# Kernel tuning notes

Hardware: AMD Instinct MI355X
Metric: run time of the kernel (lower is better)

## Reference

```python
import jax, jax.numpy as jnp
import numpy as np

B, S, D, H = 2, 2048, 1024, 16
DEPTH = D // H


def setup_inputs() -> dict:
    key = jax.random.key(0)
    ks = jax.random.split(key, 12)
    sc = 1.0 / np.sqrt(D)
    n = lambda k, shp, s=sc: jax.random.normal(k, shp, dtype=jnp.float32) * s
    return {
        "q": jax.random.normal(ks[0], (B, S, D), dtype=jnp.float32),
        "k": jax.random.normal(ks[1], (B, S, D), dtype=jnp.float32),
        "v": jax.random.normal(ks[2], (B, S, D), dtype=jnp.float32),
        # key-padding mask: 1 = masked, 0 = keep (added to logits * -1e9)
        "mask": (jax.random.uniform(ks[3], (B, 1, 1, S)) < 0.1).astype(jnp.float32),
        "wq_w": n(ks[4], (D, D)), "wq_b": jnp.zeros((D,), jnp.float32),
        "wk_w": n(ks[5], (D, D)), "wk_b": jnp.zeros((D,), jnp.float32),
        "wv_w": n(ks[6], (D, D)), "wv_b": jnp.zeros((D,), jnp.float32),
        "dense_w": n(ks[7], (D, D)), "dense_b": jnp.zeros((D,), jnp.float32),
    }


def _split_heads(x, b, s):
    # [B, S, D] -> [B, H, S, depth]
    return x.reshape(b, s, H, DEPTH).transpose(0, 2, 1, 3)


def reference(q, k, v, mask, wq_w, wq_b, wk_w, wk_b, wv_w, wv_b, dense_w, dense_b):
    b, sq, _ = q.shape
    sk = k.shape[1]
    qh = _split_heads(q @ wq_w.T + wq_b, b, sq)
    kh = _split_heads(k @ wk_w.T + wk_b, b, sk)
    vh = _split_heads(v @ wv_w.T + wv_b, b, sk)
    scale = 1.0 / jnp.sqrt(jnp.float32(DEPTH))
    logits = jnp.einsum('bhqd,bhkd->bhqk', qh, kh) * scale  # [B,H,Sq,Sk]
    logits = logits + mask * (-1e9)
    attn = jax.nn.softmax(logits, axis=-1)
    ctx = jnp.einsum('bhqk,bhkd->bhqd', attn, vh)
    ctx = ctx.transpose(0, 2, 1, 3).reshape(b, sq, D)  # concat heads
    out = ctx @ dense_w.T + dense_b
    return out, attn
```

## Files before the change

kernel.cpp:

```cpp
#include <hip/hip_runtime.h>

#define BB 2
#define SS 2048
#define DD 1024
#define HH 16
#define DEPTH 64
#define MTOT (BB*SS)
#define QW 8
#define QBLK (QW*16)
#define NT (SS/64)
#define NPROJ ((size_t)BB*HH*SS*DEPTH)
#define WSZ   ((size_t)DD*DD)

using f16 = _Float16;
typedef _Float16 f16x8 __attribute__((ext_vector_type(8)));
typedef _Float16 f16x4 __attribute__((ext_vector_type(4)));
typedef float f32x4 __attribute__((ext_vector_type(4)));

#define LOG2E 1.44269504088896f
#define SC2   (0.125f * LOG2E)

#define GLOAD16(g, l) __builtin_amdgcn_global_load_lds(                      \
    (__attribute__((address_space(1))) const void*)(g),                      \
    (__attribute__((address_space(3))) void*)(l), 16, 0, 0)

__global__ __launch_bounds__(256) void cvt_kernel(
    const float* __restrict__ q, const float* __restrict__ k, const float* __restrict__ v,
    const float* __restrict__ w0, const float* __restrict__ w1, const float* __restrict__ w2,
    f16* __restrict__ qf, f16* __restrict__ kf, f16* __restrict__ vf,
    f16* __restrict__ wq, f16* __restrict__ wk, f16* __restrict__ wv)
{
    const int z = blockIdx.y;
    const float* s = z==0?q : z==1?k : z==2?v : z==3?w0 : z==4?w1 : w2;
    f16*        d = z==0?qf: z==1?kf: z==2?vf: z==3?wq: z==4?wk: wv;
    const size_t n = (z < 3) ? NPROJ : WSZ;
    for (size_t i = ((size_t)blockIdx.x * 256 + threadIdx.x) * 8; i < n;
         i += (size_t)gridDim.x * 256 * 8) {
        f32x4 a = *(const f32x4*)(s + i);
        f32x4 b = *(const f32x4*)(s + i + 4);
        f16x8 o = {(f16)a[0], (f16)a[1], (f16)a[2], (f16)a[3],
                   (f16)b[0], (f16)b[1], (f16)b[2], (f16)b[3]};
        *(f16x8*)(d + i) = o;
    }
}

__global__ __launch_bounds__(256) void cvt2_kernel(
    const float* __restrict__ s, f16* __restrict__ d)
{
    size_t i = ((size_t)blockIdx.x * 256 + threadIdx.x) * 8;
    if (i < WSZ) {
        f32x4 a = *(const f32x4*)(s + i);
        f32x4 b = *(const f32x4*)(s + i + 4);
        f16x8 o = {(f16)a[0], (f16)a[1], (f16)a[2], (f16)a[3],
                   (f16)b[0], (f16)b[1], (f16)b[2], (f16)b[3]};
        *(f16x8*)(d + i) = o;
    }
}

__global__ __launch_bounds__(256) void proj_kernel(
    const f16* __restrict__ qf, const f16* __restrict__ kf, const f16* __restrict__ vf,
    const f16* __restrict__ wqw, const f16* __restrict__ wkw, const f16* __restrict__ wvw,
    const float* __restrict__ bq, const float* __restrict__ bk, const float* __restrict__ bv,
    f16* __restrict__ qh, f16* __restrict__ kh, f16* __restrict__ vt)
{
    const int mode = blockIdx.z;
    const f16* A    = mode==0 ? qf  : mode==1 ? kf  : vf;
    const f16* Bw   = mode==0 ? wqw : mode==1 ? wkw : wvw;
    const float* bias = mode==0 ? bq : mode==1 ? bk : bv;

    __shared__ f16 As[128*64];
    __shared__ f16 Bs[128*64];

    const int tid = threadIdx.x, wave = tid >> 6, lane = tid & 63;
    const int m0 = blockIdx.y * 128, n0 = blockIdx.x * 128;
    const int wm = (wave >> 1) * 64, wn = (wave & 1) * 64;
    const int lrow = lane & 15, g = lane >> 4;
    const int sw = lrow & 7;
    const int srow = tid >> 3;
    const int schk = (tid & 7) ^ (srow & 7);

    f32x4 acc[4][4] = {};

    for (int kk = 0; kk < DD; kk += 64) {
        #pragma unroll
        for (int i = 0; i < 4; ++i) {
            GLOAD16(A  + (size_t)(m0 + i*32 + srow) * DD + kk + schk * 8,
                    &As[i*2048 + wave*512]);
            GLOAD16(Bw + (size_t)(n0 + i*32 + srow) * DD + kk + schk * 8,
                    &Bs[i*2048 + wave*512]);
        }
        __syncthreads();
        for (int kf2 = 0; kf2 < 2; ++kf2) {
            f16x8 a[4], bf[4];
            for (int i = 0; i < 4; ++i)
                a[i]  = *(const f16x8*)&As[(wm + i*16 + lrow)*64 + ((kf2*4 + g) ^ sw)*8];
            for (int i = 0; i < 4; ++i)
                bf[i] = *(const f16x8*)&Bs[(wn + i*16 + lrow)*64 + ((kf2*4 + g) ^ sw)*8];
            for (int mi = 0; mi < 4; ++mi)
                for (int ni = 0; ni < 4; ++ni)
                    acc[mi][ni] = __builtin_amdgcn_mfma_f32_16x16x32_f16(a[mi], bf[ni], acc[mi][ni], 0, 0, 0);
        }
        __syncthreads();
    }

    const int rbase = g * 4;
    if (mode == 2) {
        for (int ni = 0; ni < 4; ++ni) {
            int n = n0 + wn + ni * 16 + lrow;
            float bval = bias[n];
            int hh = n >> 6, dep = n & 63;
            for (int mi = 0; mi < 4; ++mi) {
                int m = m0 + wm + mi * 16 + rbase;
                int bb = m >> 11, s = m & 2047;
                f16x4 pk = {(f16)(acc[mi][ni][0] + bval), (f16)(acc[mi][ni][1] + bval),
                            (f16)(acc[mi][ni][2] + bval), (f16)(acc[mi][ni][3] + bval)};
                *(f16x4*)&vt[((size_t)(bb * HH + hh) * DEPTH + dep) * SS + s] = pk;
            }
        }
    } else {
        f16* dst = (mode == 0) ? qh : kh;
        for (int ni = 0; ni < 4; ++ni) {
            int n = n0 + wn + ni * 16 + lrow;
            float bval = bias[n];
            int hh = n >> 6, dep = n & 63;
            for (int mi = 0; mi < 4; ++mi)
                for (int j = 0; j < 4; ++j) {
                    int m = m0 + wm + mi * 16 + rbase + j;
                    int bb = m >> 11, s = m & 2047;
                    dst[((size_t)(bb * HH + hh) * SS + s) * DEPTH + dep] = (f16)(acc[mi][ni][j] + bval);
                }
        }
    }
}

__global__ __launch_bounds__(512) void attn_kernel(
    const f16* __restrict__ qh, const f16* __restrict__ kh, const f16* __restrict__ vt,
    const float* __restrict__ mask, float* __restrict__ attn_out, f16* __restrict__ ctx)
{
    __shared__ float mlds[SS];
    __shared__ f16 Ks[2][64*64];
    __shared__ f16 Vs[2][64*64];
    __shared__ f16 Pl[QW][16][72];

    const int tid = threadIdx.x, wave = tid >> 6, lane = tid & 63;
    const int L = blockIdx.x;
    const int xcd = L & 7, iw = L >> 3;
    const int bh = xcd * 4 + (iw >> 4);
    const int qb = iw & 15;
    const int b = bh >> 4, h = bh & 15;
    const int q0 = qb * QBLK;
    const int lrow = lane & 15, g = lane >> 4;
    const int rbase = g * 4;
    const int sw = lrow & 7;
    const int srow = tid >> 3;
    const int schk = (tid & 7) ^ (srow & 7);

    const f16* Qbase = qh + (size_t)bh * SS * DEPTH;
    const f16* Kb = kh + (size_t)bh * SS * DEPTH;
    const f16* Vb = vt + (size_t)bh * DEPTH * SS;

    for (int i = tid; i < SS; i += 512) mlds[i] = mask[b * SS + i] * (-1e9f * LOG2E);

    f16x8 aq[2];
    for (int kf2 = 0; kf2 < 2; ++kf2)
        aq[kf2] = *(const f16x8*)(Qbase + (size_t)(q0 + wave*16 + lrow) * DEPTH + kf2*32 + g*8);

    float s_l[4] = {0.f, 0.f, 0.f, 0.f};
    GLOAD16(Kb + (size_t)(0*64 + srow) * DEPTH + schk * 8, &Ks[0][wave * 512]);
    __syncthreads();
    for (int kt = 0; kt < NT; ++kt) {
        const int cur = kt & 1;
        if (kt + 1 < NT)
            GLOAD16(Kb + (size_t)((kt+1)*64 + srow) * DEPTH + schk * 8, &Ks[cur ^ 1][wave * 512]);
        for (int nf = 0; nf < 4; ++nf) {
            f32x4 a4 = {};
            for (int kf2 = 0; kf2 < 2; ++kf2) {
                f16x8 bf = *(const f16x8*)&Ks[cur][(nf*16 + lrow)*64 + ((kf2*4 + g) ^ sw)*8];
                a4 = __builtin_amdgcn_mfma_f32_16x16x32_f16(aq[kf2], bf, a4, 0, 0, 0);
            }
            float mb = mlds[kt*64 + nf*16 + lrow];
            for (int j = 0; j < 4; ++j)
                s_l[j] += __builtin_amdgcn_exp2f(a4[j] * SC2 + mb);
        }
        __syncthreads();
    }
    for (int j = 0; j < 4; ++j) {
        float s = s_l[j];
        for (int off = 1; off < 16; off <<= 1) s += __shfl_xor(s, off);
        s_l[j] = 1.0f / s;
    }

    f32x4 cacc[4] = {};
    float* arow = attn_out + ((size_t)bh * SS + q0 + wave * 16) * SS;
    GLOAD16(Kb + (size_t)(0*64 + srow) * DEPTH + schk * 8, &Ks[0][wave * 512]);
    GLOAD16(Vb + (size_t)srow * SS + 0*64 + schk * 8,      &Vs[0][wave * 512]);
    __syncthreads();
    for (int kt = 0; kt < NT; ++kt) {
        const int cur = kt & 1;
        if (kt + 1 < NT) {
            GLOAD16(Kb + (size_t)((kt+1)*64 + srow) * DEPTH + schk * 8, &Ks[cur ^ 1][wave * 512]);
            GLOAD16(Vb + (size_t)srow * SS + (kt+1)*64 + schk * 8,      &Vs[cur ^ 1][wave * 512]);
        }
        for (int nf = 0; nf < 4; ++nf) {
            f32x4 a4 = {};
            for (int kf2 = 0; kf2 < 2; ++kf2) {
                f16x8 bf = *(const f16x8*)&Ks[cur][(nf*16 + lrow)*64 + ((kf2*4 + g) ^ sw)*8];
                a4 = __builtin_amdgcn_mfma_f32_16x16x32_f16(aq[kf2], bf, a4, 0, 0, 0);
            }
            float mb = mlds[kt*64 + nf*16 + lrow];
            for (int j = 0; j < 4; ++j) {
                float p = __builtin_amdgcn_exp2f(a4[j] * SC2 + mb) * s_l[j];
                Pl[wave][rbase + j][nf*16 + lrow] = (f16)p;
            }
        }
        for (int i = 0; i < 4; ++i) {
            int r = i * 4 + g;
            f16x4 pv4 = *(const f16x4*)&Pl[wave][r][lrow * 4];
            f32x4 o = {(float)pv4[0], (float)pv4[1], (float)pv4[2], (float)pv4[3]};
            __builtin_nontemporal_store(o, (f32x4*)&arow[(size_t)r * SS + kt*64 + lrow*4]);
        }
        for (int kf2 = 0; kf2 < 2; ++kf2) {
            f16x8 pa = *(const f16x8*)&Pl[wave][lrow][kf2*32 + g*8];
            for (int nf = 0; nf < 4; ++nf) {
                f16x8 bv = *(const f16x8*)&Vs[cur][(nf*16 + lrow)*64 + ((kf2*4 + g) ^ sw)*8];
                cacc[nf] = __builtin_amdgcn_mfma_f32_16x16x32_f16(pa, bv, cacc[nf], 0, 0, 0);
            }
        }
        __syncthreads();
    }
    for (int nf = 0; nf < 4; ++nf)
        for (int j = 0; j < 4; ++j) {
            int qrow = q0 + wave * 16 + rbase + j;
            ctx[((size_t)(b * SS + qrow) * HH + h) * DEPTH + nf*16 + lrow] = (f16)cacc[nf][j];
        }
}

__global__ __launch_bounds__(256) void dense_kernel(
    const f16* __restrict__ ctx, const f16* __restrict__ W16,
    const float* __restrict__ bias, float* __restrict__ out)
{
    __shared__ f16 As[128*64];
    __shared__ f16 Bs[128*64];

    const int tid = threadIdx.x, wave = tid >> 6, lane = tid & 63;
    const int m0 = blockIdx.y * 128, n0 = blockIdx.x * 128;
    const int wm = (wave >> 1) * 64, wn = (wave & 1) * 64;
    const int lrow = lane & 15, g = lane >> 4;
    const int sw = lrow & 7;
    const int srow = tid >> 3;
    const int schk = (tid & 7) ^ (srow & 7);

    f32x4 acc[4][4] = {};

    for (int kk = 0; kk < DD; kk += 64) {
        #pragma unroll
        for (int i = 0; i < 4; ++i) {
            GLOAD16(ctx + (size_t)(m0 + i*32 + srow) * DD + kk + schk * 8,
                    &As[i*2048 + wave*512]);
            GLOAD16(W16 + (size_t)(n0 + i*32 + srow) * DD + kk + schk * 8,
                    &Bs[i*2048 + wave*512]);
        }
        __syncthreads();
        for (int kf2 = 0; kf2 < 2; ++kf2) {
            f16x8 a[4], bf[4];
            for (int i = 0; i < 4; ++i)
                a[i]  = *(const f16x8*)&As[(wm + i*16 + lrow)*64 + ((kf2*4 + g) ^ sw)*8];
            for (int i = 0; i < 4; ++i)
                bf[i] = *(const f16x8*)&Bs[(wn + i*16 + lrow)*64 + ((kf2*4 + g) ^ sw)*8];
            for (int mi = 0; mi < 4; ++mi)
                for (int ni = 0; ni < 4; ++ni)
                    acc[mi][ni] = __builtin_amdgcn_mfma_f32_16x16x32_f16(a[mi], bf[ni], acc[mi][ni], 0, 0, 0);
        }
        __syncthreads();
    }

    const int rbase = g * 4;
    for (int ni = 0; ni < 4; ++ni) {
        int n = n0 + wn + ni * 16 + lrow;
        float bval = bias[n];
        for (int mi = 0; mi < 4; ++mi)
            for (int j = 0; j < 4; ++j) {
                int m = m0 + wm + mi * 16 + rbase + j;
                out[(size_t)m * DD + n] = acc[mi][ni][j] + bval;
            }
    }
}

extern "C" void kernel_launch(void* const* d_in, const int* in_sizes, int n_in,
                              void* d_out, int out_size, void* d_ws, size_t ws_size,
                              hipStream_t stream) {
    const float* q       = (const float*)d_in[0];
    const float* k       = (const float*)d_in[1];
    const float* v       = (const float*)d_in[2];
    const float* mask    = (const float*)d_in[3];
    const float* wq_w    = (const float*)d_in[4];
    const float* wq_b    = (const float*)d_in[5];
    const float* wk_w    = (const float*)d_in[6];
    const float* wk_b    = (const float*)d_in[7];
    const float* wv_w    = (const float*)d_in[8];
    const float* wv_b    = (const float*)d_in[9];
    const float* dense_w = (const float*)d_in[10];
    const float* dense_b = (const float*)d_in[11];

    float* out  = (float*)d_out;
    float* attn = out + (size_t)MTOT * DD;

    f16* qh  = (f16*)d_ws;
    f16* kh  = qh + NPROJ;
    f16* vt  = kh + NPROJ;
    f16* ctx = vt + NPROJ;

    f16* sc   = (f16*)attn;
    f16* qf   = sc;
    f16* kf   = sc + NPROJ;
    f16* vf   = sc + 2*NPROJ;
    f16* wq16 = sc + 3*NPROJ;
    f16* wk16 = wq16 + WSZ;
    f16* wv16 = wk16 + WSZ;

    f16* dw16 = qh;

    cvt_kernel<<<dim3(1024, 6), 256, 0, stream>>>(q, k, v, wq_w, wk_w, wv_w,
                                                  qf, kf, vf, wq16, wk16, wv16);
    proj_kernel<<<dim3(8, 32, 3), 256, 0, stream>>>(qf, kf, vf, wq16, wk16, wv16,
                                                    wq_b, wk_b, wv_b, qh, kh, vt);
    attn_kernel<<<dim3(512), 512, 0, stream>>>(qh, kh, vt, mask, attn, ctx);
    cvt2_kernel<<<dim3(512), 256, 0, stream>>>(dense_w, dw16);
    dense_kernel<<<dim3(8, 32), 256, 0, stream>>>(ctx, dw16, dense_b, out);
}
```

Baseline: 235.6 us.

## Double-buffer GEMM K-tiles and defer attention-probability stores by one tile

The projection and dense GEMMs switch from single-buffered 64-wide K tiles to double-buffered 32-wide K tiles with a new XOR swizzle. The next tile's async global-to-LDS load is issued before computing on the current one, so load latency overlaps the MFMA work. In the attention kernel, the fp32 attention-probability stores for a tile are held in registers and issued at the start of the next iteration, so they overlap the following loads and MFMAs. The cost is more registers, a barrier every 32 K instead of every 64, and a swizzle change that must still avoid LDS bank conflicts.

Measured after the change: 244.0 us. +3.6%, slower.

```diff
diff --git a/kernel.cpp b/kernel.cpp
--- a/kernel.cpp
+++ b/kernel.cpp
@@ -68,38 +68,45 @@
     const f16* Bw   = mode==0 ? wqw : mode==1 ? wkw : wvw;
     const float* bias = mode==0 ? bq : mode==1 ? bk : bv;
 
-    __shared__ f16 As[128*64];
-    __shared__ f16 Bs[128*64];
+    __shared__ f16 As[2][128*32];
+    __shared__ f16 Bs[2][128*32];
 
     const int tid = threadIdx.x, wave = tid >> 6, lane = tid & 63;
     const int m0 = blockIdx.y * 128, n0 = blockIdx.x * 128;
     const int wm = (wave >> 1) * 64, wn = (wave & 1) * 64;
     const int lrow = lane & 15, g = lane >> 4;
-    const int sw = lrow & 7;
-    const int srow = tid >> 3;
-    const int schk = (tid & 7) ^ (srow & 7);
+    const int swr = (lrow >> 1) & 3;
+    const int srow = tid >> 2;
+    const int schk = (tid & 3) ^ ((tid >> 3) & 3);
 
     f32x4 acc[4][4] = {};
 
-    for (int kk = 0; kk < DD; kk += 64) {
-        #pragma unroll
-        for (int i = 0; i < 4; ++i) {
-            GLOAD16(A  + (size_t)(m0 + i*32 + srow) * DD + kk + schk * 8,
-                    &As[i*2048 + wave*512]);
-            GLOAD16(Bw + (size_t)(n0 + i*32 + srow) * DD + kk + schk * 8,
-                    &Bs[i*2048 + wave*512]);
-        }
-        __syncthreads();
-        for (int kf2 = 0; kf2 < 2; ++kf2) {
-            f16x8 a[4], bf[4];
-            for (int i = 0; i < 4; ++i)
-                a[i]  = *(const f16x8*)&As[(wm + i*16 + lrow)*64 + ((kf2*4 + g) ^ sw)*8];
-            for (int i = 0; i < 4; ++i)
-                bf[i] = *(const f16x8*)&Bs[(wn + i*16 + lrow)*64 + ((kf2*4 + g) ^ sw)*8];
-            for (int mi = 0; mi < 4; ++mi)
-                for (int ni = 0; ni < 4; ++ni)
-                    acc[mi][ni] = __builtin_amdgcn_mfma_f32_16x16x32_f16(a[mi], bf[ni], acc[mi][ni], 0, 0, 0);
-        }
+    auto stage = [&](int t, int buf) {
+        const int kk = t * 32;
+        #pragma unroll
+        for (int s2 = 0; s2 < 2; ++s2) {
+            GLOAD16(A  + (size_t)(m0 + s2*64 + srow) * DD + kk + schk * 8,
+                    &As[buf][s2*2048 + wave*512]);
+            GLOAD16(Bw + (size_t)(n0 + s2*64 + srow) * DD + kk + schk * 8,
+                    &Bs[buf][s2*2048 + wave*512]);
+        }
+    };
+
+    stage(0, 0);
+    __syncthreads();
+    for (int t = 0; t < DD/32; ++t) {
+        const int cur = t & 1;
+        if (t + 1 < DD/32) stage(t + 1, cur ^ 1);
+        f16x8 a[4], bf[4];
+        #pragma unroll
+        for (int i = 0; i < 4; ++i)
+            a[i]  = *(const f16x8*)&As[cur][(wm + i*16 + lrow)*32 + (g ^ swr)*8];
+        #pragma unroll
+        for (int i = 0; i < 4; ++i)
+            bf[i] = *(const f16x8*)&Bs[cur][(wn + i*16 + lrow)*32 + (g ^ swr)*8];
+        for (int mi = 0; mi < 4; ++mi)
+            for (int ni = 0; ni < 4; ++ni)
+                acc[mi][ni] = __builtin_amdgcn_mfma_f32_16x16x32_f16(a[mi], bf[ni], acc[mi][ni], 0, 0, 0);
         __syncthreads();
     }
 
@@ -191,12 +198,21 @@
     }
 
     f32x4 cacc[4] = {};
+    f32x4 st[4];
     float* arow = attn_out + ((size_t)bh * SS + q0 + wave * 16) * SS;
     GLOAD16(Kb + (size_t)(0*64 + srow) * DEPTH + schk * 8, &Ks[0][wave * 512]);
     GLOAD16(Vb + (size_t)srow * SS + 0*64 + schk * 8,      &Vs[0][wave * 512]);
     __syncthreads();
     for (int kt = 0; kt < NT; ++kt) {
         const int cur = kt & 1;
+        if (kt > 0) {
+            #pragma unroll
+            for (int i = 0; i < 4; ++i) {
+                int r = i * 4 + g;
+                __builtin_nontemporal_store(st[i],
+                    (f32x4*)&arow[(size_t)r * SS + (kt-1)*64 + lrow*4]);
+            }
+        }
         if (kt + 1 < NT) {
             GLOAD16(Kb + (size_t)((kt+1)*64 + srow) * DEPTH + schk * 8, &Ks[cur ^ 1][wave * 512]);
             GLOAD16(Vb + (size_t)srow * SS + (kt+1)*64 + schk * 8,      &Vs[cur ^ 1][wave * 512]);
@@ -213,12 +229,6 @@
                 Pl[wave][rbase + j][nf*16 + lrow] = (f16)p;
             }
         }
-        for (int i = 0; i < 4; ++i) {
-            int r = i * 4 + g;
-            f16x4 pv4 = *(const f16x4*)&Pl[wave][r][lrow * 4];
-            f32x4 o = {(float)pv4[0], (float)pv4[1], (float)pv4[2], (float)pv4[3]};
-            __builtin_nontemporal_store(o, (f32x4*)&arow[(size_t)r * SS + kt*64 + lrow*4]);
-        }
         for (int kf2 = 0; kf2 < 2; ++kf2) {
             f16x8 pa = *(const f16x8*)&Pl[wave][lrow][kf2*32 + g*8];
             for (int nf = 0; nf < 4; ++nf) {
@@ -226,7 +236,19 @@
                 cacc[nf] = __builtin_amdgcn_mfma_f32_16x16x32_f16(pa, bv, cacc[nf], 0, 0, 0);
             }
         }
+        #pragma unroll
+        for (int i = 0; i < 4; ++i) {
+            int r = i * 4 + g;
+            f16x4 pv4 = *(const f16x4*)&Pl[wave][r][lrow * 4];
+            st[i] = (f32x4){(float)pv4[0], (float)pv4[1], (float)pv4[2], (float)pv4[3]};
+        }
         __syncthreads();
+    }
+    #pragma unroll
+    for (int i = 0; i < 4; ++i) {
+        int r = i * 4 + g;
+        __builtin_nontemporal_store(st[i],
+            (f32x4*)&arow[(size_t)r * SS + (NT-1)*64 + lrow*4]);
     }
     for (int nf = 0; nf < 4; ++nf)
         for (int j = 0; j < 4; ++j) {
@@ -239,38 +261,45 @@
     const f16* __restrict__ ctx, const f16* __restrict__ W16,
     const float* __restrict__ bias, float* __restrict__ out)
 {
-    __shared__ f16 As[128*64];
-    __shared__ f16 Bs[128*64];
+    __shared__ f16 As[2][128*32];
+    __shared__ f16 Bs[2][128*32];
 
     const int tid = threadIdx.x, wave = tid >> 6, lane = tid & 63;
     const int m0 = blockIdx.y * 128, n0 = blockIdx.x * 128;
     const int wm = (wave >> 1) * 64, wn = (wave & 1) * 64;
     const int lrow = lane & 15, g = lane >> 4;
-    const int sw = lrow & 7;
-    const int srow = tid >> 3;
-    const int schk = (tid & 7) ^ (srow & 7);
+    const int swr = (lrow >> 1) & 3;
+    const int srow = tid >> 2;
+    const int schk = (tid & 3) ^ ((tid >> 3) & 3);
 
     f32x4 acc[4][4] = {};
 
-    for (int kk = 0; kk < DD; kk += 64) {
-        #pragma unroll
-        for (int i = 0; i < 4; ++i) {
-            GLOAD16(ctx + (size_t)(m0 + i*32 + srow) * DD + kk + schk * 8,
-                    &As[i*2048 + wave*512]);
-            GLOAD16(W16 + (size_t)(n0 + i*32 + srow) * DD + kk + schk * 8,
-                    &Bs[i*2048 + wave*512]);
-        }
-        __syncthreads();
-        for (int kf2 = 0; kf2 < 2; ++kf2) {
-            f16x8 a[4], bf[4];
-            for (int i = 0; i < 4; ++i)
-                a[i]  = *(const f16x8*)&As[(wm + i*16 + lrow)*64 + ((kf2*4 + g) ^ sw)*8];
-            for (int i = 0; i < 4; ++i)
-                bf[i] = *(const f16x8*)&Bs[(wn + i*16 + lrow)*64 + ((kf2*4 + g) ^ sw)*8];
-            for (int mi = 0; mi < 4; ++mi)
-                for (int ni = 0; ni < 4; ++ni)
-                    acc[mi][ni] = __builtin_amdgcn_mfma_f32_16x16x32_f16(a[mi], bf[ni], acc[mi][ni], 0, 0, 0);
-        }
+    auto stage = [&](int t, int buf) {
+        const int kk = t * 32;
+        #pragma unroll
+        for (int s2 = 0; s2 < 2; ++s2) {
+            GLOAD16(ctx + (size_t)(m0 + s2*64 + srow) * DD + kk + schk * 8,
+                    &As[buf][s2*2048 + wave*512]);
+            GLOAD16(W16 + (size_t)(n0 + s2*64 + srow) * DD + kk + schk * 8,
+                    &Bs[buf][s2*2048 + wave*512]);
+        }
+    };
+
+    stage(0, 0);
+    __syncthreads();
+    for (int t = 0; t < DD/32; ++t) {
+        const int cur = t & 1;
+        if (t + 1 < DD/32) stage(t + 1, cur ^ 1);
+        f16x8 a[4], bf[4];
+        #pragma unroll
+        for (int i = 0; i < 4; ++i)
+            a[i]  = *(const f16x8*)&As[cur][(wm + i*16 + lrow)*32 + (g ^ swr)*8];
+        #pragma unroll
+        for (int i = 0; i < 4; ++i)
+            bf[i] = *(const f16x8*)&Bs[cur][(wn + i*16 + lrow)*32 + (g ^ swr)*8];
+        for (int mi = 0; mi < 4; ++mi)
+            for (int ni = 0; ni < 4; ++ni)
+                acc[mi][ni] = __builtin_amdgcn_mfma_f32_16x16x32_f16(a[mi], bf[ni], acc[mi][ni], 0, 0, 0);
         __syncthreads();
     }
 
```

## Defer attention-probability stores one tile and shrink mask to byte flags

Applied to the files above, without the earlier changes.

The attention kernel now reads each tile's probabilities back from LDS after the PV MFMAs into registers, and issues the fp32 nontemporal global stores at the start of the next iteration, so the HBM writes overlap the following tile's compute. The fp32 mask bias array in LDS is replaced by a byte flag array with a multiplicative 0/1 select, which cuts LDS use. The launch bounds also gain a min-blocks hint of 6, which pressures register allocation. The deferred stores keep 16 extra registers live, and masked positions give exactly zero instead of exp of a huge negative value. That matches the reference in practice, though rows with every key masked would behave differently.

Result: no change. 235.2 us (-0.2%).

```diff
diff --git a/kernel.cpp b/kernel.cpp
--- a/kernel.cpp
+++ b/kernel.cpp
@@ -133,11 +133,11 @@
     }
 }
 
-__global__ __launch_bounds__(512) void attn_kernel(
+__global__ __launch_bounds__(512, 6) void attn_kernel(
     const f16* __restrict__ qh, const f16* __restrict__ kh, const f16* __restrict__ vt,
     const float* __restrict__ mask, float* __restrict__ attn_out, f16* __restrict__ ctx)
 {
-    __shared__ float mlds[SS];
+    __shared__ unsigned char mflag[SS];
     __shared__ f16 Ks[2][64*64];
     __shared__ f16 Vs[2][64*64];
     __shared__ f16 Pl[QW][16][72];
@@ -159,7 +159,8 @@
     const f16* Kb = kh + (size_t)bh * SS * DEPTH;
     const f16* Vb = vt + (size_t)bh * DEPTH * SS;
 
-    for (int i = tid; i < SS; i += 512) mlds[i] = mask[b * SS + i] * (-1e9f * LOG2E);
+    for (int i = tid; i < SS; i += 512)
+        mflag[i] = mask[b * SS + i] > 0.5f ? 1 : 0;
 
     f16x8 aq[2];
     for (int kf2 = 0; kf2 < 2; ++kf2)
@@ -178,9 +179,9 @@
                 f16x8 bf = *(const f16x8*)&Ks[cur][(nf*16 + lrow)*64 + ((kf2*4 + g) ^ sw)*8];
                 a4 = __builtin_amdgcn_mfma_f32_16x16x32_f16(aq[kf2], bf, a4, 0, 0, 0);
             }
-            float mb = mlds[kt*64 + nf*16 + lrow];
+            float sel = mflag[kt*64 + nf*16 + lrow] ? 0.f : 1.f;
             for (int j = 0; j < 4; ++j)
-                s_l[j] += __builtin_amdgcn_exp2f(a4[j] * SC2 + mb);
+                s_l[j] += sel * __builtin_amdgcn_exp2f(a4[j] * SC2);
         }
         __syncthreads();
     }
@@ -191,12 +192,21 @@
     }
 
     f32x4 cacc[4] = {};
+    f32x4 st[4];
     float* arow = attn_out + ((size_t)bh * SS + q0 + wave * 16) * SS;
     GLOAD16(Kb + (size_t)(0*64 + srow) * DEPTH + schk * 8, &Ks[0][wave * 512]);
     GLOAD16(Vb + (size_t)srow * SS + 0*64 + schk * 8,      &Vs[0][wave * 512]);
     __syncthreads();
     for (int kt = 0; kt < NT; ++kt) {
         const int cur = kt & 1;
+        if (kt > 0) {
+            #pragma unroll
+            for (int i = 0; i < 4; ++i) {
+                int r = i * 4 + g;
+                __builtin_nontemporal_store(st[i],
+                    (f32x4*)&arow[(size_t)r * SS + (kt-1)*64 + lrow*4]);
+            }
+        }
         if (kt + 1 < NT) {
             GLOAD16(Kb + (size_t)((kt+1)*64 + srow) * DEPTH + schk * 8, &Ks[cur ^ 1][wave * 512]);
             GLOAD16(Vb + (size_t)srow * SS + (kt+1)*64 + schk * 8,      &Vs[cur ^ 1][wave * 512]);
@@ -207,17 +217,11 @@
                 f16x8 bf = *(const f16x8*)&Ks[cur][(nf*16 + lrow)*64 + ((kf2*4 + g) ^ sw)*8];
                 a4 = __builtin_amdgcn_mfma_f32_16x16x32_f16(aq[kf2], bf, a4, 0, 0, 0);
             }
-            float mb = mlds[kt*64 + nf*16 + lrow];
+            float sel = mflag[kt*64 + nf*16 + lrow] ? 0.f : 1.f;
             for (int j = 0; j < 4; ++j) {
-                float p = __builtin_amdgcn_exp2f(a4[j] * SC2 + mb) * s_l[j];
+                float p = sel * __builtin_amdgcn_exp2f(a4[j] * SC2) * s_l[j];
                 Pl[wave][rbase + j][nf*16 + lrow] = (f16)p;
             }
-        }
-        for (int i = 0; i < 4; ++i) {
-            int r = i * 4 + g;
-            f16x4 pv4 = *(const f16x4*)&Pl[wave][r][lrow * 4];
-            f32x4 o = {(float)pv4[0], (float)pv4[1], (float)pv4[2], (float)pv4[3]};
-            __builtin_nontemporal_store(o, (f32x4*)&arow[(size_t)r * SS + kt*64 + lrow*4]);
         }
         for (int kf2 = 0; kf2 < 2; ++kf2) {
             f16x8 pa = *(const f16x8*)&Pl[wave][lrow][kf2*32 + g*8];
@@ -226,7 +230,19 @@
                 cacc[nf] = __builtin_amdgcn_mfma_f32_16x16x32_f16(pa, bv, cacc[nf], 0, 0, 0);
             }
         }
-        __syncthreads();
+        #pragma unroll
+        for (int i = 0; i < 4; ++i) {
+            int r = i * 4 + g;
+            f16x4 pv4 = *(const f16x4*)&Pl[wave][r][lrow * 4];
+            st[i] = (f32x4){(float)pv4[0], (float)pv4[1], (float)pv4[2], (float)pv4[3]};
+        }
+        __syncthreads();
+    }
+    #pragma unroll
+    for (int i = 0; i < 4; ++i) {
+        int r = i * 4 + g;
+        __builtin_nontemporal_store(st[i],
+            (f32x4*)&arow[(size_t)r * SS + (NT-1)*64 + lrow*4]);
     }
     for (int nf = 0; nf < 4; ++nf)
         for (int j = 0; j < 4; ++j) {
```
